# Optimization experiments

Measured on AMD Instinct MI355X. Metric: run time of the kernel, lower is better.

Reference implementation:

```python
import jax, jax.numpy as jnp
import numpy as np

B, T, F, H = 512, 365, 16, 256


def _lstm_layer(x, W_ih, W_hh, b_ih, b_hh):
    """batch_first LSTM layer, torch gate order (i, f, g, o).
    x: [B, T, in]. Returns (outputs [B, T, H], final h [B, H])."""
    # Precompute input projections for all timesteps: [T, B, 4H]
    x_proj = jnp.einsum('bti,gi->tbg', x, W_ih) + (b_ih + b_hh)
    h0 = jnp.zeros((x.shape[0], W_hh.shape[1]), x.dtype)
    c0 = jnp.zeros_like(h0)

    def step(carry, xp):
        h, c = carry
        z = xp + h @ W_hh.T  # [B, 4H]
        i, f, g, o = jnp.split(z, 4, axis=-1)
        c = jax.nn.sigmoid(f) * c + jax.nn.sigmoid(i) * jnp.tanh(g)
        h = jax.nn.sigmoid(o) * jnp.tanh(c)
        return (h, c), h

    (hT, _), hs = jax.lax.scan(step, (h0, c0), x_proj)
    return jnp.transpose(hs, (1, 0, 2)), hT


def setup_inputs() -> dict:
    key = jax.random.key(0)
    ks = jax.random.split(key, 11)
    s1 = 1.0 / np.sqrt(H)
    u = lambda k, shape: jax.random.uniform(k, shape, jnp.float32, -s1, s1)
    return {
        'x': jax.random.normal(ks[0], (B, T, F), jnp.float32),
        'W_ih1': u(ks[1], (4 * H, F)),
        'W_hh1': u(ks[2], (4 * H, H)),
        'b_ih1': u(ks[3], (4 * H,)),
        'b_hh1': u(ks[4], (4 * H,)),
        'W_ih2': u(ks[5], (4 * H, H)),
        'W_hh2': u(ks[6], (4 * H, H)),
        'b_ih2': u(ks[7], (4 * H,)),
        'b_hh2': u(ks[8], (4 * H,)),
        'W_lin': u(ks[9], (1, H)),
        'b_lin': u(ks[10], (1,)),
    }


def reference(x, W_ih1, W_hh1, b_ih1, b_hh1, W_ih2, W_hh2, b_ih2, b_hh2, W_lin, b_lin):
    h1_seq, _ = _lstm_layer(x, W_ih1, W_hh1, b_ih1, b_hh1)
    # dropout(p=0.1) is identity in eval mode
    _, hT = _lstm_layer(h1_seq, W_ih2, W_hh2, b_ih2, b_hh2)
    out = (hT @ W_lin.T + b_lin).reshape(-1)  # [B]
    return out
```

## Files before the change

### kernel.cpp

```cpp
#include <hip/hip_runtime.h>


#define T_STEPS 365
#define XSTR 36

typedef __attribute__((ext_vector_type(8))) short short8;
typedef __attribute__((ext_vector_type(4))) float float4_;
typedef __attribute__((ext_vector_type(4))) unsigned int uint4_;
typedef unsigned long long u64;
typedef unsigned int u32;

#define MFMA16(a, b, c) __builtin_amdgcn_mfma_f32_16x16x32_bf16((a), (b), (c), 0, 0, 0)
#define LD64(p) __hip_atomic_load((p), __ATOMIC_RELAXED, __HIP_MEMORY_SCOPE_AGENT)

__device__ __forceinline__ unsigned short f2bf(float v) {
    union { float f; u32 u; } a; a.f = v;
    u32 r = a.u + 0x7fffu + ((a.u >> 16) & 1u);
    return (unsigned short)(r >> 16);
}
__device__ __forceinline__ float bf2f(unsigned short h) {
    union { u32 u; float f; } a; a.u = ((u32)h) << 16; return a.f;
}
__device__ __forceinline__ u32 packhl(float v) {
    unsigned short hi = f2bf(v);
    unsigned short lo = f2bf(v - bf2f(hi));
    return ((u32)hi << 16) | (u32)lo;
}
__device__ __forceinline__ float sigm(float x)  { return 1.f / (1.f + __expf(-x)); }
__device__ __forceinline__ float tanh_(float x) { return 2.f / (1.f + __expf(-2.f * x)) - 1.f; }

__device__ __forceinline__ void unpk(uint4_ a, uint4_ b, short8& hi, short8& lo) {
    union U { u32 d[4]; short8 s; } H, L;
    H.d[0] = __builtin_amdgcn_perm(a.y, a.x, 0x07060302u);
    H.d[1] = __builtin_amdgcn_perm(a.w, a.z, 0x07060302u);
    H.d[2] = __builtin_amdgcn_perm(b.y, b.x, 0x07060302u);
    H.d[3] = __builtin_amdgcn_perm(b.w, b.z, 0x07060302u);
    L.d[0] = __builtin_amdgcn_perm(a.y, a.x, 0x05040100u);
    L.d[1] = __builtin_amdgcn_perm(a.w, a.z, 0x05040100u);
    L.d[2] = __builtin_amdgcn_perm(b.y, b.x, 0x05040100u);
    L.d[3] = __builtin_amdgcn_perm(b.w, b.z, 0x05040100u);
    hi = H.s; lo = L.s;
}

__global__ void prep_w(
    const float* __restrict__ Wih1, const float* __restrict__ Whh1,
    const float* __restrict__ bih1, const float* __restrict__ bhh1,
    const float* __restrict__ Wih2, const float* __restrict__ Whh2,
    const float* __restrict__ bih2, const float* __restrict__ bhh2,
    unsigned short* __restrict__ w1h, unsigned short* __restrict__ w1l,
    unsigned short* __restrict__ w2h, unsigned short* __restrict__ w2l,
    float* __restrict__ bias1, float* __restrict__ bias2)
{
    const int tile = blockIdx.x;
    const int g = tile >> 4, ns = tile & 15;
    const int tid = threadIdx.x;

    for (int idx = tid; idx < 9 * 512; idx += 256) {
        int ks = idx >> 9, off = idx & 511, r = off >> 5, kk = off & 31;
        int R = g * 256 + ns * 16 + r;
        float v;
        if (ks < 8)       v = Whh1[R * 256 + ks * 32 + kk];
        else if (kk < 16) v = Wih1[R * 16 + kk];
        else              v = 0.f;
        unsigned short h = f2bf(v);
        size_t d = (size_t)(tile * 9 + ks) * 512 + off;
        w1h[d] = h; w1l[d] = f2bf(v - bf2f(h));
    }
    for (int idx = tid; idx < 16 * 512; idx += 256) {
        int ks = idx >> 9, off = idx & 511, r = off >> 5, kk = off & 31;
        int R = g * 256 + ns * 16 + r;
        int k = ks * 32 + kk;
        float v = (k < 256) ? Wih2[R * 256 + k] : Whh2[R * 256 + (k - 256)];
        unsigned short h = f2bf(v);
        size_t d = (size_t)(tile * 16 + ks) * 512 + off;
        w2h[d] = h; w2l[d] = f2bf(v - bf2f(h));
    }
    if (tid < 16) {
        int R = g * 256 + ns * 16 + tid;
        bias1[R] = bih1[R] + bhh1[R];
        bias2[R] = bih2[R] + bhh2[R];
    }
}


__global__ __launch_bounds__(512, 2) void lstm_main(
    const float* __restrict__ x,
    const unsigned short* __restrict__ w1h, const unsigned short* __restrict__ w1l,
    const unsigned short* __restrict__ w2h, const unsigned short* __restrict__ w2l,
    const float* __restrict__ bias1, const float* __restrict__ bias2,
    u32* hb1, u32* hb2, u32* prog,
    const float* __restrict__ Wlin, const float* __restrict__ blin,
    float* __restrict__ out)
{
    __shared__ __align__(16) u32 xbuf[32 * XSTR];
    __shared__ __align__(16) float zb1[3 * 64 * 36];
    __shared__ __align__(16) float zb2[5 * 64 * 36];
    __shared__ __align__(16) float hp[32][17];

    const int tid  = threadIdx.x;
    const int lane = tid & 63;
    const int wv   = tid >> 6;
    const int quad = lane >> 4;
    const int r16  = lane & 15;
    const int bg   = blockIdx.x & 15;
    const int ns   = blockIdx.x >> 4;

    u32* myprog = prog + bg * 64;

    const bool isL1 = (wv < 3);
    int s0, s1, s2, s3;
    if      (wv == 0) { s0 = 0;  s1 = 1;  s2 = 2;  s3 = -1; }
    else if (wv == 1) { s0 = 3;  s1 = 4;  s2 = 5;  s3 = -1; }
    else if (wv == 2) { s0 = 6;  s1 = 7;  s2 = 8;  s3 = -1; }
    else if (wv == 3) { s0 = 0;  s1 = 1;  s2 = 2;  s3 = 3;  }
    else if (wv == 4) { s0 = 4;  s1 = 5;  s2 = 6;  s3 = -1; }
    else if (wv == 5) { s0 = 7;  s1 = 8;  s2 = 9;  s3 = -1; }
    else if (wv == 6) { s0 = 10; s1 = 11; s2 = 12; s3 = -1; }
    else              { s0 = 13; s1 = 14; s2 = 15; s3 = -1; }

    const int loff = r16 * 32 + quad * 8;
    const unsigned short* WHsrc = isL1 ? w1h : w2h;
    const unsigned short* WLsrc = isL1 ? w1l : w2l;
    const int NK = isL1 ? 9 : 16;
    short8 WH[4][4], WL[4][4];
#pragma unroll
    for (int s = 0; s < 4; s++) {
        const int b = (s == 0) ? s0 : (s == 1) ? s1 : (s == 2) ? s2 : s3;
#pragma unroll
        for (int g = 0; g < 4; g++) {
            if (b >= 0) {
                size_t off = ((size_t)((g * 16 + ns) * NK + b)) * 512 + loff;
                WH[g][s] = *(const short8*)(WHsrc + off);
                WL[g][s] = *(const short8*)(WLsrc + off);
            } else {
                WH[g][s] = short8{0,0,0,0,0,0,0,0};
                WL[g][s] = short8{0,0,0,0,0,0,0,0};
            }
        }
    }

    float bi[4] = {0.f, 0.f, 0.f, 0.f};
    if (tid < 256) {
        const float* bsrc = (tid < 128) ? bias1 : bias2;
        int colg = ns * 16 + (tid & 15);
#pragma unroll
        for (int g = 0; g < 4; g++) bi[g] = bsrc[g * 256 + colg];
    }
    float cst[4] = {0.f, 0.f, 0.f, 0.f};

    for (int i = tid; i < 32 * XSTR; i += 512) xbuf[i] = 0u;
    __syncthreads();
    {
        int row = tid >> 4, col = tid & 15;
        float v = x[((size_t)(bg * 32 + row) * T_STEPS + 0) * 16 + col];
        xbuf[row * XSTR + col] = packhl(v);
    }
    __syncthreads();

#define ISSUE(Fv, sid) do {                                                   \
        if ((sid) >= 0 && !(isL1 && (sid) == 8)) {                            \
            const u64* bp_ = (isL1 || (sid) < 8) ? h1base : h2base;           \
            int kb_ = (isL1 || (sid) < 8) ? (sid) : ((sid) - 8);              \
            const u64* a_ = bp_ + (size_t)kb_ * 512 + (size_t)quad * 128      \
                                + (size_t)r16 * 2;                            \
            Fv[0] = LD64(a_ + 0);  Fv[1] = LD64(a_ + 1);                      \
            Fv[2] = LD64(a_ + 64); Fv[3] = LD64(a_ + 65);                     \
            Fv[4] = LD64(a_ + 32); Fv[5] = LD64(a_ + 33);                     \
            Fv[6] = LD64(a_ + 96); Fv[7] = LD64(a_ + 97);                     \
        } } while (0)

#define PROC(Fv, sid, sreg) do {                                              \
        if ((sid) >= 0) {                                                     \
            uint4_ q00, q01, q10, q11;                                        \
            if (isL1 && (sid) == 8) {                                         \
                q00 = *(const uint4_*)&xbuf[r16 * XSTR + quad * 8];           \
                q01 = *(const uint4_*)&xbuf[r16 * XSTR + quad * 8 + 4];       \
                q10 = *(const uint4_*)&xbuf[(16 + r16) * XSTR + quad * 8];    \
                q11 = *(const uint4_*)&xbuf[(16 + r16) * XSTR + quad * 8 + 4];\
            } else {                                                          \
                union { u64 q[2]; uint4_ v; } u0_, u1_, u2_, u3_;             \
                u0_.q[0] = Fv[0]; u0_.q[1] = Fv[1]; q00 = u0_.v;              \
                u1_.q[0] = Fv[2]; u1_.q[1] = Fv[3]; q01 = u1_.v;              \
                u2_.q[0] = Fv[4]; u2_.q[1] = Fv[5]; q10 = u2_.v;              \
                u3_.q[0] = Fv[6]; u3_.q[1] = Fv[7]; q11 = u3_.v;              \
            }                                                                 \
            short8 ah0, al0, ah1, al1;                                        \
            unpk(q00, q01, ah0, al0);                                         \
            unpk(q10, q11, ah1, al1);                                         \
            _Pragma("unroll")                                                 \
            for (int g = 0; g < 4; g++) {                                     \
                acc[g][0] = MFMA16(ah0, WH[g][sreg], acc[g][0]);              \
                acc[g][0] = MFMA16(al0, WH[g][sreg], acc[g][0]);              \
                acc[g][0] = MFMA16(ah0, WL[g][sreg], acc[g][0]);              \
                acc[g][1] = MFMA16(ah1, WH[g][sreg], acc[g][1]);              \
                acc[g][1] = MFMA16(al1, WH[g][sreg], acc[g][1]);              \
                acc[g][1] = MFMA16(ah1, WL[g][sreg], acc[g][1]);              \
            }                                                                 \
        } } while (0)

    for (int t = 0; t <= T_STEPS; t++) {
        const int p = t & 1;

        {
            const u32 tgt = (u32)t;
            while (__hip_atomic_load(&myprog[lane], __ATOMIC_RELAXED,
                                     __HIP_MEMORY_SCOPE_AGENT) < tgt)
                __builtin_amdgcn_s_sleep(1);
        }
        __syncthreads();

        const u64* h1base = (const u64*)hb1 + (size_t)((1 - p) * 16 + bg) * 4096;
        const u64* h2base = (const u64*)hb2 + (size_t)(p * 16 + bg) * 4096;

        float4_ acc[4][2];
        const float4_ z4 = {0.f, 0.f, 0.f, 0.f};
#pragma unroll
        for (int g = 0; g < 4; g++) { acc[g][0] = z4; acc[g][1] = z4; }

        u64 F0[8], F1[8];
        ISSUE(F0, s0); ISSUE(F1, s1);
        PROC(F0, s0, 0); ISSUE(F0, s2);
        PROC(F1, s1, 1); ISSUE(F1, s3);
        PROC(F0, s2, 2);
        PROC(F1, s3, 3);

        {
            float* zbase = isL1 ? (zb1 + wv * (64 * 36)) : (zb2 + (wv - 3) * (64 * 36));
#pragma unroll
            for (int g = 0; g < 4; g++)
#pragma unroll
                for (int rt = 0; rt < 2; rt++)
                    *(float4_*)&zbase[(size_t)(g * 16 + r16) * 36 + rt * 16 + quad * 4] = acc[g][rt];
        }
        __syncthreads();

        if (tid < 256) {
            const bool is1 = (tid < 128);
            const int hcol = tid & 15;
            const int rq   = (tid >> 4) & 7;
            const float* zb = is1 ? zb1 : zb2;
            const int np = is1 ? 3 : 5;
            float4_ z[4];
#pragma unroll
            for (int g = 0; g < 4; g++) {
                float4_ s = {bi[g], bi[g], bi[g], bi[g]};
#pragma unroll
                for (int pw = 0; pw < 5; pw++) {
                    if (pw < np)
                        s += *(const float4_*)&zb[(size_t)(pw * 64 + g * 16 + hcol) * 36 + rq * 4];
                }
                z[g] = s;
            }
            u32* hb = is1 ? hb1 : hb2;
            const int slot = is1 ? p : (1 - p);
            const int gc = ns * 16 + hcol;
            const size_t ob = (size_t)(slot * 16 + bg) * 8192
                            + (gc >> 5) * 1024 + ((gc >> 3) & 3) * 256
                            + ((gc >> 2) & 1) * 128 + rq * 16 + (gc & 3);
#pragma unroll
            for (int j = 0; j < 4; j++) {
                float zi = z[0][j], zf = z[1][j], zg = z[2][j], zo = z[3][j];
                float nc = sigm(zf) * cst[j] + sigm(zi) * tanh_(zg);
                float h  = sigm(zo) * tanh_(nc);
                if (!is1 && t == 0) { nc = 0.f; h = 0.f; }
                cst[j] = nc;
                __hip_atomic_store(&hb[ob + (size_t)j * 4], packhl(h),
                                   __ATOMIC_RELAXED, __HIP_MEMORY_SCOPE_WORKGROUP);
            }
            asm volatile("s_waitcnt vmcnt(0)" ::: "memory");
            if (lane == 0)
                __hip_atomic_store(&myprog[ns * 4 + wv], (u32)(t + 1),
                                   __ATOMIC_RELAXED, __HIP_MEMORY_SCOPE_WORKGROUP);
        } else {
            const int i0 = tid - 256;
            const int tn = (t + 1 <= T_STEPS - 1) ? (t + 1) : (T_STEPS - 1);
#pragma unroll
            for (int k = 0; k < 2; k++) {
                int idx = i0 + 256 * k;
                int row = idx >> 4, col = idx & 15;
                float v = x[((size_t)(bg * 32 + row) * T_STEPS + tn) * 16 + col];
                xbuf[row * XSTR + col] = packhl(v);
            }
        }
    }

    if (ns != 0) return;
    {
        const u32 tgt = (u32)(T_STEPS + 1);
        while (__hip_atomic_load(&myprog[lane], __ATOMIC_RELAXED,
                                 __HIP_MEMORY_SCOPE_AGENT) < tgt)
            __builtin_amdgcn_s_sleep(1);
    }
    {
        int row = tid >> 4, seg = tid & 15;
        const size_t sb = (size_t)(0 * 16 + bg) * 8192;
        float s = 0.f;
#pragma unroll
        for (int j = 0; j < 16; j++) {
            int gc = seg * 16 + j;
            size_t idx = sb + (gc >> 5) * 1024 + ((gc >> 3) & 3) * 256
                       + ((gc >> 2) & 1) * 128 + row * 4 + (gc & 3);
            u32 v = __hip_atomic_load(&hb2[idx], __ATOMIC_RELAXED, __HIP_MEMORY_SCOPE_AGENT);
            s += (bf2f((unsigned short)(v >> 16)) + bf2f((unsigned short)v)) * Wlin[seg * 16 + j];
        }
        hp[row][seg] = s;
    }
    __syncthreads();
    if (tid < 32) {
        float s = 0.f;
#pragma unroll
        for (int j = 0; j < 16; j++) s += hp[tid][j];
        out[bg * 32 + tid] = s + blin[0];
    }
}

extern "C" void kernel_launch(void* const* d_in, const int* in_sizes, int n_in,
                              void* d_out, int out_size, void* d_ws, size_t ws_size,
                              hipStream_t stream) {
    const float* x    = (const float*)d_in[0];
    const float* Wih1 = (const float*)d_in[1];
    const float* Whh1 = (const float*)d_in[2];
    const float* bih1 = (const float*)d_in[3];
    const float* bhh1 = (const float*)d_in[4];
    const float* Wih2 = (const float*)d_in[5];
    const float* Whh2 = (const float*)d_in[6];
    const float* bih2 = (const float*)d_in[7];
    const float* bhh2 = (const float*)d_in[8];
    const float* Wlin = (const float*)d_in[9];
    const float* blin = (const float*)d_in[10];
    float* out = (float*)d_out;

    char* pp = (char*)d_ws;
    unsigned short* w1h = (unsigned short*)pp; pp += (size_t)64 * 9 * 512 * 2;
    unsigned short* w1l = (unsigned short*)pp; pp += (size_t)64 * 9 * 512 * 2;
    unsigned short* w2h = (unsigned short*)pp; pp += (size_t)64 * 16 * 512 * 2;
    unsigned short* w2l = (unsigned short*)pp; pp += (size_t)64 * 16 * 512 * 2;
    float* bias1 = (float*)pp; pp += 1024 * 4;
    float* bias2 = (float*)pp; pp += 1024 * 4;
    char* zero_base = pp;
    u32* hb1 = (u32*)pp; pp += (size_t)2 * 16 * 8192 * 4;
    u32* hb2 = (u32*)pp; pp += (size_t)2 * 16 * 8192 * 4;
    u32* prog = (u32*)pp; pp += 16 * 64 * 4;
    size_t zero_bytes = (size_t)(pp - zero_base);

    hipMemsetAsync(zero_base, 0, zero_bytes, stream);
    prep_w<<<64, 256, 0, stream>>>(Wih1, Whh1, bih1, bhh1, Wih2, Whh2, bih2, bhh2,
                                   w1h, w1l, w2h, w2l, bias1, bias2);
    lstm_main<<<256, 512, 0, stream>>>(x, w1h, w1l, w2h, w2l, bias1, bias2,
                                       hb1, hb2, prog, Wlin, blin, out);
}
```

Baseline: 1.812 ms.

## Replace per-step block barrier with targeted flag waits and direct x loads

Each wave now spins only on the progress flags of the producer blocks whose h slices it actually consumes. This replaces the all-lane poll followed by a block-wide barrier at the top of every timestep. The shared x staging buffer is removed: layer-1 waves load x for the current step straight from global memory into registers and pack it. A third fetch register set lets three h slices be in flight at once. The extra flag waits before the zb writes and before the cell update keep the timesteps ordered without the first barrier, at the cost of more complex cross-block synchronisation and more registers.

```diff
diff --git a/kernel.cpp b/kernel.cpp
--- a/kernel.cpp
+++ b/kernel.cpp
@@ -2,7 +2,6 @@
 
 
 #define T_STEPS 365
-#define XSTR 36
 
 typedef __attribute__((ext_vector_type(8))) short short8;
 typedef __attribute__((ext_vector_type(4))) float float4_;
@@ -92,7 +91,6 @@
     const float* __restrict__ Wlin, const float* __restrict__ blin,
     float* __restrict__ out)
 {
-    __shared__ __align__(16) u32 xbuf[32 * XSTR];
     __shared__ __align__(16) float zb1[3 * 64 * 36];
     __shared__ __align__(16) float zb2[5 * 64 * 36];
     __shared__ __align__(16) float hp[32][17];
@@ -148,14 +146,17 @@
     }
     float cst[4] = {0.f, 0.f, 0.f, 0.f};
 
-    for (int i = tid; i < 32 * XSTR; i += 512) xbuf[i] = 0u;
-    __syncthreads();
+    int fi = -1;
     {
-        int row = tid >> 4, col = tid & 15;
-        float v = x[((size_t)(bg * 32 + row) * T_STEPS + 0) * 16 + col];
-        xbuf[row * XSTR + col] = packhl(v);
-    }
-    __syncthreads();
+        int sl = (quad == 0) ? s0 : (quad == 1) ? s1 : (quad == 2) ? s2 : s3;
+        int sub = lane & 15;
+        if (sl >= 0 && sub < 4 && !(isL1 && sl == 8)) {
+            bool ish2 = (!isL1 && sl >= 8);
+            int blk = ish2 ? (sl - 8) : sl;
+            fi = (2 * blk + (sub & 1)) * 4 + ((sub >> 1) & 1) + (ish2 ? 2 : 0);
+        }
+    }
+    const int zbflag = ns * 4 + (isL1 ? 0 : 2);
 
 #define ISSUE(Fv, sid) do {                                                   \
         if ((sid) >= 0 && !(isL1 && (sid) == 8)) {                            \
@@ -171,22 +172,14 @@
 
 #define PROC(Fv, sid, sreg) do {                                              \
         if ((sid) >= 0) {                                                     \
-            uint4_ q00, q01, q10, q11;                                        \
-            if (isL1 && (sid) == 8) {                                         \
-                q00 = *(const uint4_*)&xbuf[r16 * XSTR + quad * 8];           \
-                q01 = *(const uint4_*)&xbuf[r16 * XSTR + quad * 8 + 4];       \
-                q10 = *(const uint4_*)&xbuf[(16 + r16) * XSTR + quad * 8];    \
-                q11 = *(const uint4_*)&xbuf[(16 + r16) * XSTR + quad * 8 + 4];\
-            } else {                                                          \
-                union { u64 q[2]; uint4_ v; } u0_, u1_, u2_, u3_;             \
-                u0_.q[0] = Fv[0]; u0_.q[1] = Fv[1]; q00 = u0_.v;              \
-                u1_.q[0] = Fv[2]; u1_.q[1] = Fv[3]; q01 = u1_.v;              \
-                u2_.q[0] = Fv[4]; u2_.q[1] = Fv[5]; q10 = u2_.v;              \
-                u3_.q[0] = Fv[6]; u3_.q[1] = Fv[7]; q11 = u3_.v;              \
-            }                                                                 \
+            union { u64 q[2]; uint4_ v; } u0_, u1_, u2_, u3_;                 \
+            u0_.q[0] = Fv[0]; u0_.q[1] = Fv[1];                               \
+            u1_.q[0] = Fv[2]; u1_.q[1] = Fv[3];                               \
+            u2_.q[0] = Fv[4]; u2_.q[1] = Fv[5];                               \
+            u3_.q[0] = Fv[6]; u3_.q[1] = Fv[7];                               \
             short8 ah0, al0, ah1, al1;                                        \
-            unpk(q00, q01, ah0, al0);                                         \
-            unpk(q10, q11, ah1, al1);                                         \
+            unpk(u0_.v, u1_.v, ah0, al0);                                     \
+            unpk(u2_.v, u3_.v, ah1, al1);                                     \
             _Pragma("unroll")                                                 \
             for (int g = 0; g < 4; g++) {                                     \
                 acc[g][0] = MFMA16(ah0, WH[g][sreg], acc[g][0]);              \
@@ -203,11 +196,10 @@
 
         {
             const u32 tgt = (u32)t;
-            while (__hip_atomic_load(&myprog[lane], __ATOMIC_RELAXED,
-                                     __HIP_MEMORY_SCOPE_AGENT) < tgt)
+            while (fi >= 0 && __hip_atomic_load(&myprog[fi], __ATOMIC_RELAXED,
+                                                __HIP_MEMORY_SCOPE_AGENT) < tgt)
                 __builtin_amdgcn_s_sleep(1);
         }
-        __syncthreads();
 
         const u64* h1base = (const u64*)hb1 + (size_t)((1 - p) * 16 + bg) * 4096;
         const u64* h2base = (const u64*)hb2 + (size_t)(p * 16 + bg) * 4096;
@@ -217,15 +209,44 @@
 #pragma unroll
         for (int g = 0; g < 4; g++) { acc[g][0] = z4; acc[g][1] = z4; }
 
-        u64 F0[8], F1[8];
-        ISSUE(F0, s0); ISSUE(F1, s1);
-        PROC(F0, s0, 0); ISSUE(F0, s2);
-        PROC(F1, s1, 1); ISSUE(F1, s3);
-        PROC(F0, s2, 2);
-        PROC(F1, s3, 3);
+        u64 F0[8], F1[8], F2[8];
+        ISSUE(F0, s0); ISSUE(F1, s1); ISSUE(F2, s2);
+
+        if (isL1 && s2 == 8) {
+            if (quad < 2) {
+                int tt = (t < T_STEPS) ? t : (T_STEPS - 1);
+                const float* xp0 = x + ((size_t)(bg * 32 + r16) * T_STEPS + tt) * 16 + quad * 8;
+                const float* xp1 = xp0 + (size_t)16 * T_STEPS * 16;
+                float4_ a0 = *(const float4_*)xp0, a1 = *(const float4_*)(xp0 + 4);
+                float4_ b0 = *(const float4_*)xp1, b1 = *(const float4_*)(xp1 + 4);
+                F2[0] = (u64)packhl(a0.x) | ((u64)packhl(a0.y) << 32);
+                F2[1] = (u64)packhl(a0.z) | ((u64)packhl(a0.w) << 32);
+                F2[2] = (u64)packhl(a1.x) | ((u64)packhl(a1.y) << 32);
+                F2[3] = (u64)packhl(a1.z) | ((u64)packhl(a1.w) << 32);
+                F2[4] = (u64)packhl(b0.x) | ((u64)packhl(b0.y) << 32);
+                F2[5] = (u64)packhl(b0.z) | ((u64)packhl(b0.w) << 32);
+                F2[6] = (u64)packhl(b1.x) | ((u64)packhl(b1.y) << 32);
+                F2[7] = (u64)packhl(b1.z) | ((u64)packhl(b1.w) << 32);
+            } else {
+#pragma unroll
+                for (int i = 0; i < 8; i++) F2[i] = 0;
+            }
+        }
+
+        PROC(F0, s0, 0);
+        ISSUE(F0, s3);
+        PROC(F1, s1, 1);
+        PROC(F2, s2, 2);
+        PROC(F0, s3, 3);
 
         {
-            float* zbase = isL1 ? (zb1 + wv * (64 * 36)) : (zb2 + (wv - 3) * (64 * 36));
+            const u32 tgt = (u32)t;
+            while (lane < 2 && __hip_atomic_load(&myprog[zbflag + lane], __ATOMIC_RELAXED,
+                                                 __HIP_MEMORY_SCOPE_AGENT) < tgt)
+                __builtin_amdgcn_s_sleep(1);
+        }
+        {
+            float* zbase = isL1 ? (zb1 + wv * 2304) : (zb2 + (wv - 3) * 2304);
 #pragma unroll
             for (int g = 0; g < 4; g++)
 #pragma unroll
@@ -235,6 +256,12 @@
         __syncthreads();
 
         if (tid < 256) {
+            {
+                const u32 tgt = (u32)t;
+                while (__hip_atomic_load(&myprog[lane], __ATOMIC_RELAXED,
+                                         __HIP_MEMORY_SCOPE_AGENT) < tgt)
+                    __builtin_amdgcn_s_sleep(1);
+            }
             const bool is1 = (tid < 128);
             const int hcol = tid & 15;
             const int rq   = (tid >> 4) & 7;
@@ -271,16 +298,6 @@
             if (lane == 0)
                 __hip_atomic_store(&myprog[ns * 4 + wv], (u32)(t + 1),
                                    __ATOMIC_RELAXED, __HIP_MEMORY_SCOPE_WORKGROUP);
-        } else {
-            const int i0 = tid - 256;
-            const int tn = (t + 1 <= T_STEPS - 1) ? (t + 1) : (T_STEPS - 1);
-#pragma unroll
-            for (int k = 0; k < 2; k++) {
-                int idx = i0 + 256 * k;
-                int row = idx >> 4, col = idx & 15;
-                float v = x[((size_t)(bg * 32 + row) * T_STEPS + tn) * 16 + col];
-                xbuf[row * XSTR + col] = packhl(v);
-            }
         }
     }
 
@@ -291,6 +308,7 @@
                                  __HIP_MEMORY_SCOPE_AGENT) < tgt)
             __builtin_amdgcn_s_sleep(1);
     }
+    __syncthreads();
     {
         int row = tid >> 4, seg = tid & 15;
         const size_t sb = (size_t)(0 * 16 + bg) * 8192;
```

Measured after the change: 2.051 ms. 1.13x slower.
